# Performance work log

Measured on AMD Instinct MI355X. Metric: run time of the kernel, lower is better.

Reference implementation:

```python
import jax, jax.numpy as jnp
import numpy as np

E2M1_GRID = jnp.array([0.0, 0.5, 1.0, 1.5, 2.0, 3.0, 4.0, 6.0], dtype=jnp.float32)
E2M1_MIDS = (E2M1_GRID[1:] + E2M1_GRID[:-1]) / 2.0
FP4_MAX = 6.0
FP8_E4M3_MAX = 448.0


def nvfp4_quant_dequant(w):
    # Emulates tetrajetv2.quant_fp4_dequant_trans_fused: two-level scaling
    # (fp32 outer scale per 128 inputs, fp8-e4m3 inner scale per 16 inputs),
    # values rounded to the signed E2M1 grid, then dequantized.
    O, I = w.shape
    w16 = w.reshape(O, I // 128, 8, 16)
    amax128 = jnp.max(jnp.abs(w16), axis=(-2, -1))          # [O, I/128]
    outer = amax128 / (FP4_MAX * FP8_E4M3_MAX)
    outer = jnp.where(outer > 0, outer, 1.0)
    amax16 = jnp.max(jnp.abs(w16), axis=-1)                  # [O, I/128, 8]
    inner = amax16 / FP4_MAX / outer[..., None]
    inner = inner.astype(jnp.float8_e4m3fn).astype(jnp.float32)  # fp8 round
    scale = outer[..., None] * inner                          # [O, I/128, 8]
    safe = jnp.where(scale > 0, scale, 1.0)[..., None]
    code = w16 / safe
    a = jnp.abs(code)
    idx = jnp.searchsorted(E2M1_MIDS, a)                      # nearest grid pt
    q = E2M1_GRID[idx] * jnp.sign(code)
    return (q * scale[..., None]).reshape(O, I)


def setup_inputs() -> dict:
    key = jax.random.key(0)
    k0, k1, k2 = jax.random.split(key, 3)
    B, S, H = 2, 2048, 2048
    hidden_states = jax.random.normal(k0, (B, S, H), dtype=jnp.float32)
    # raw weights ~ N(0, 0.023) as in FP4Linear init, then fake-quantized
    w_qkv = jax.random.normal(k1, (3 * H, H), dtype=jnp.float32) * 0.023
    w_o = jax.random.normal(k2, (H, H), dtype=jnp.float32) * 0.023
    w_qkv = nvfp4_quant_dequant(w_qkv)
    w_o = nvfp4_quant_dequant(w_o)
    return {"hidden_states": hidden_states, "w_qkv": w_qkv, "w_o": w_o}


def reference(hidden_states, w_qkv, w_o):
    B, S, H = hidden_states.shape
    num_heads = 16
    head_dim = H // num_heads
    qkv = jnp.einsum('bsh,oh->bso', hidden_states, w_qkv)      # [B,S,3H]
    qkv = qkv.reshape(B, S, 3, num_heads, head_dim)
    qkv = jnp.transpose(qkv, (2, 0, 3, 1, 4))                  # [3,B,nh,S,hd]
    q, k, v = qkv[0], qkv[1], qkv[2]
    scale = 1.0 / jnp.sqrt(jnp.float32(head_dim))
    scores = jnp.einsum('bhqd,bhkd->bhqk', q, k) * scale
    causal = jnp.tril(jnp.ones((S, S), dtype=bool))
    scores = jnp.where(causal, scores, jnp.finfo(scores.dtype).min)
    probs = jax.nn.softmax(scores, axis=-1)
    attn = jnp.einsum('bhqk,bhkd->bhqd', probs, v)             # [B,nh,S,hd]
    attn = jnp.transpose(attn, (0, 2, 1, 3)).reshape(B, S, H)
    return jnp.einsum('bsh,oh->bso', attn, w_o)
```

## Files before the change

kernel.cpp:

```cpp
#include <hip/hip_runtime.h>
#include <hip/hip_bf16.h>
#include <stdint.h>

typedef __bf16 bf16x8 __attribute__((ext_vector_type(8)));
typedef float f32x4 __attribute__((ext_vector_type(4)));

#define AS1 __attribute__((address_space(1)))
#define AS3 __attribute__((address_space(3)))

#define PBAR() do { __builtin_amdgcn_sched_barrier(0); asm volatile("s_barrier" ::: "memory"); __builtin_amdgcn_sched_barrier(0); } while (0)
#define LGK0() do { asm volatile("s_waitcnt lgkmcnt(0)" ::: "memory"); __builtin_amdgcn_sched_barrier(0); } while (0)
#define VMCNT(n) do { asm volatile("s_waitcnt vmcnt(" #n ")" ::: "memory"); __builtin_amdgcn_sched_barrier(0); } while (0)

__device__ __forceinline__ unsigned short f2bf(float x) {
    union { float f; uint32_t u; } v; v.f = x;
    uint32_t r = v.u + 0x7fffu + ((v.u >> 16) & 1u);
    return (unsigned short)(r >> 16);
}

__global__ void k_f2bf(const float* __restrict__ in, unsigned short* __restrict__ out, int n4) {
    int i = blockIdx.x * blockDim.x + threadIdx.x;
    if (i >= n4) return;
    float4 v = reinterpret_cast<const float4*>(in)[i];
    ushort4 o;
    o.x = f2bf(v.x); o.y = f2bf(v.y); o.z = f2bf(v.z); o.w = f2bf(v.w);
    reinterpret_cast<ushort4*>(out)[i] = o;
}

template <typename TOUT>
__global__ __launch_bounds__(512, 2) void k_gemm128x256(
    const unsigned short* __restrict__ A,
    const unsigned short* __restrict__ B,
    TOUT* __restrict__ C, int M, int N, int K, int ngrid)
{
    __shared__ __align__(16) unsigned short Albuf[3][4096];
    __shared__ __align__(16) unsigned short Blbuf[3][8192];
    const int tid = threadIdx.x, lane = tid & 63, wv = tid >> 6;
    const int wr = wv >> 2, wc = wv & 3;
    const int fl = lane & 15, fg = lane >> 4;
    const int cpx = ngrid >> 3;
    const int sw = ((int)blockIdx.x & 7) * cpx + ((int)blockIdx.x >> 3);
    const int bm = sw & 31, bn = sw >> 5;
    const int nK = K >> 5;

    const unsigned short* Ag = A + (size_t)bm * 128 * K;
    const unsigned short* Bg = B + (size_t)bn * 256 * K;

    auto stageA = [&](int buf, int t) {
        const int r = tid >> 2;
        const int cs = (tid & 3) ^ ((r >> 1) & 3);
        const unsigned short* src = Ag + (size_t)r * K + t * 32 + cs * 8;
        __builtin_amdgcn_global_load_lds((const AS1 void*)src,
            (AS3 void*)((char*)&Albuf[buf][0] + wv * 1024), 16, 0, 0);
    };
    auto stageB = [&](int buf, int half, int t) {
        const int r = tid >> 2;
        const int cs = (tid & 3) ^ ((r >> 1) & 3);
        const unsigned short* src = Bg + (size_t)(half * 128 + r) * K + t * 32 + cs * 8;
        __builtin_amdgcn_global_load_lds((const AS1 void*)src,
            (AS3 void*)((char*)&Blbuf[buf][0] + half * 8192 + wv * 1024), 16, 0, 0);
    };
    auto ldfrag = [&](const unsigned short* base, int r) -> bf16x8 {
        return *reinterpret_cast<const bf16x8*>(
            (const char*)base + r * 64 + ((fg ^ ((r >> 1) & 3)) << 4));
    };

    f32x4 acc[4][4];
#pragma unroll
    for (int i = 0; i < 4; ++i)
#pragma unroll
        for (int j = 0; j < 4; ++j) acc[i][j] = (f32x4){0.f, 0.f, 0.f, 0.f};

    stageA(0, 0); stageB(0, 0, 0); stageB(0, 1, 0);
    stageA(1, 1); stageB(1, 0, 1); stageB(1, 1, 1);
    asm volatile("s_waitcnt vmcnt(3)" ::: "memory");
    PBAR();

    int c = 0;
    for (int t = 0; t < nK; ++t) {
        const unsigned short* Ac = Albuf[c];
        const unsigned short* Bc = Blbuf[c];
        bf16x8 af[4], bv[4];
#pragma unroll
        for (int i = 0; i < 4; ++i) af[i] = ldfrag(Ac, wr * 64 + i * 16 + fl);
#pragma unroll
        for (int j = 0; j < 4; ++j) bv[j] = ldfrag(Bc, wc * 64 + j * 16 + fl);
        if (t + 2 < nK) {
            int nb = c + 2; if (nb >= 3) nb -= 3;
            stageA(nb, t + 2); stageB(nb, 0, t + 2); stageB(nb, 1, t + 2);
        }
        PBAR();
        LGK0();
        __builtin_amdgcn_s_setprio(1);
#pragma unroll
        for (int i = 0; i < 4; ++i)
#pragma unroll
            for (int j = 0; j < 4; ++j)
                acc[i][j] = __builtin_amdgcn_mfma_f32_16x16x32_bf16(af[i], bv[j], acc[i][j], 0, 0, 0);
        __builtin_amdgcn_s_setprio(0);
        if (t + 2 < nK)      { asm volatile("s_waitcnt vmcnt(3)" ::: "memory"); }
        else if (t + 1 < nK) { asm volatile("s_waitcnt vmcnt(0)" ::: "memory"); }
        PBAR();
        ++c; if (c == 3) c = 0;
    }

#pragma unroll
    for (int i = 0; i < 4; ++i)
#pragma unroll
        for (int j = 0; j < 4; ++j)
#pragma unroll
            for (int r = 0; r < 4; ++r) {
                int row = bm * 128 + wr * 64 + i * 16 + fg * 4 + r;
                int col = bn * 256 + wc * 64 + j * 16 + fl;
                float v = acc[i][j][r];
                if constexpr (sizeof(TOUT) == 2)
                    ((unsigned short*)C)[(size_t)row * N + col] = f2bf(v);
                else
                    C[(size_t)row * N + col] = v;
            }
}

__global__ void k_transpose_v(const unsigned short* __restrict__ qkv, unsigned short* __restrict__ vT) {
    __shared__ unsigned short t[32][33];
    const int bh = blockIdx.z;
    const int b = bh >> 4, h = bh & 15;
    const int s0 = blockIdx.x * 32, d0 = blockIdx.y * 32;
    const int tx = threadIdx.x, ty = threadIdx.y;
#pragma unroll
    for (int i = 0; i < 4; ++i) {
        int s = s0 + ty + i * 8;
        t[ty + i * 8][tx] = qkv[(size_t)(b * 2048 + s) * 6144 + 4096 + h * 128 + d0 + tx];
    }
    __syncthreads();
#pragma unroll
    for (int i = 0; i < 4; ++i) {
        int d = d0 + ty + i * 8;
        vT[((size_t)bh * 128 + d) * 2048 + s0 + tx] = t[tx][ty + i * 8];
    }
}

__global__ __launch_bounds__(256, 2) void k_attn(
    const unsigned short* __restrict__ qkv, const unsigned short* __restrict__ vT,
    unsigned short* __restrict__ out)
{
    __shared__ unsigned short Klds[2][8192];
    __shared__ unsigned short Vlds[8192];
    __shared__ __align__(16) unsigned short Plds[4][2048];

    const int tid = threadIdx.x, lane = tid & 63, wv = tid >> 6;
    const int fl = lane & 15, fg = lane >> 4;
    const int bh = blockIdx.y;
    const int qb = (bh >= 16) ? blockIdx.x : 15 - blockIdx.x;
    const int b = bh >> 4, h = bh & 15;
    const int q0w = qb * 128 + wv * 32;
    const size_t base = (size_t)b * 2048 * 6144 + (size_t)h * 128;
    const unsigned short* Qbase = qkv + base;
    const unsigned short* Kbase = qkv + base + 2048;
    const unsigned short* Vbase = vT + (size_t)bh * 128 * 2048;
    unsigned short* pw = Plds[wv];

    bf16x8 qf[2][4];
#pragma unroll
    for (int m = 0; m < 2; ++m)
#pragma unroll
        for (int kk = 0; kk < 4; ++kk)
            qf[m][kk] = *reinterpret_cast<const bf16x8*>(
                Qbase + (size_t)(q0w + m * 16 + fl) * 6144 + kk * 32 + fg * 8);
    asm volatile("s_waitcnt vmcnt(0)" ::: "memory");
    __builtin_amdgcn_sched_barrier(0);

    auto stageK = [&](int buf, int kv0) {
#pragma unroll
        for (int rnd = 0; rnd < 4; ++rnd) {
            int ch = rnd * 256 + tid;
            int row = ch >> 4;
            int cbl = ((ch & 15) << 4) ^ ((row & 7) << 4);
            const unsigned short* src = Kbase + (size_t)(kv0 + row) * 6144 + (cbl >> 1);
            __builtin_amdgcn_global_load_lds((const AS1 void*)src,
                (AS3 void*)((char*)&Klds[buf][0] + (rnd * 256 + wv * 64) * 16), 16, 0, 0);
        }
    };
    auto stageV = [&](int kv0) {
#pragma unroll
        for (int rnd = 0; rnd < 4; ++rnd) {
            int ch = rnd * 256 + tid;
            int row = ch >> 3;
            int cbl = ((ch & 7) << 4) ^ ((row & 7) << 4);
            const unsigned short* src = Vbase + (size_t)row * 2048 + kv0 + (cbl >> 1);
            __builtin_amdgcn_global_load_lds((const AS1 void*)src,
                (AS3 void*)((char*)&Vlds[0] + (rnd * 256 + wv * 64) * 16), 16, 0, 0);
        }
    };

    f32x4 acc[2][8];
#pragma unroll
    for (int m = 0; m < 2; ++m)
#pragma unroll
        for (int nb = 0; nb < 8; ++nb) acc[m][nb] = (f32x4){0.f, 0.f, 0.f, 0.f};
    float l_r[2] = {0.f, 0.f};
    const float sc = 0.08838834764831845f;
    const int nIter = 2 * qb + 2;

    stageK(0, 0);

    for (int it = 0; it < nIter; ++it) {
        const int kv0 = it * 64;
        const bool act = (kv0 <= q0w + 31);
        const bool haveK = (it + 1 < nIter);
        stageV(kv0);
        if (haveK) stageK((it + 1) & 1, kv0 + 64);
        __builtin_amdgcn_sched_barrier(0);
        if (haveK) { VMCNT(8); } else { VMCNT(4); }
        PBAR();
        if (act) {
            const bool full = (kv0 + 63 <= q0w);
            const unsigned short* Kb = Klds[it & 1];
            f32x4 s[2][4];
#pragma unroll
            for (int m = 0; m < 2; ++m)
#pragma unroll
                for (int n = 0; n < 4; ++n) s[m][n] = (f32x4){0.f, 0.f, 0.f, 0.f};
            __builtin_amdgcn_s_setprio(1);
#pragma unroll
            for (int kk = 0; kk < 4; ++kk)
#pragma unroll
                for (int n = 0; n < 4; ++n) {
                    const int row = n * 16 + fl;
                    bf16x8 kf = *reinterpret_cast<const bf16x8*>(
                        (const char*)Kb + row * 256 + ((kk * 64 + fg * 16) ^ ((row & 7) << 4)));
                    s[0][n] = __builtin_amdgcn_mfma_f32_16x16x32_bf16(kf, qf[0][kk], s[0][n], 0, 0, 0);
                    s[1][n] = __builtin_amdgcn_mfma_f32_16x16x32_bf16(kf, qf[1][kk], s[1][n], 0, 0, 0);
                }
            __builtin_amdgcn_s_setprio(0);
#pragma unroll
            for (int m = 0; m < 2; ++m) {
                const int qi = q0w + m * 16 + fl;
                const int prow = m * 16 + fl;
                const int rb = prow * 128, swz = (prow & 7) << 4;
#pragma unroll
                for (int n = 0; n < 4; ++n) {
                    const int kbase = kv0 + n * 16 + fg * 4;
                    float v0 = s[m][n][0] * sc, v1 = s[m][n][1] * sc,
                          v2 = s[m][n][2] * sc, v3 = s[m][n][3] * sc;
                    if (!full) {
                        if (kbase     > qi) v0 = -3e38f;
                        if (kbase + 1 > qi) v1 = -3e38f;
                        if (kbase + 2 > qi) v2 = -3e38f;
                        if (kbase + 3 > qi) v3 = -3e38f;
                    }
                    float p0 = __expf(v0 - 10.f), p1 = __expf(v1 - 10.f),
                          p2 = __expf(v2 - 10.f), p3 = __expf(v3 - 10.f);
                    l_r[m] += p0 + p1 + p2 + p3;
                    uint32_t lo = (uint32_t)f2bf(p0) | ((uint32_t)f2bf(p1) << 16);
                    uint32_t hi = (uint32_t)f2bf(p2) | ((uint32_t)f2bf(p3) << 16);
                    const int byte = rb + ((n * 32 + fg * 8) ^ swz);
                    uint2 pk; pk.x = lo; pk.y = hi;
                    *reinterpret_cast<uint2*>((char*)pw + byte) = pk;
                }
            }
            LGK0();
        }
        if (haveK) { VMCNT(4); } else { VMCNT(0); }
        PBAR();
        if (act) {
            bf16x8 pf[2][2];
#pragma unroll
            for (int m = 0; m < 2; ++m)
#pragma unroll
                for (int k2 = 0; k2 < 2; ++k2) {
                    const int row = m * 16 + fl;
                    pf[m][k2] = *reinterpret_cast<const bf16x8*>(
                        (const char*)pw + row * 128 + ((k2 * 64 + fg * 16) ^ ((row & 7) << 4)));
                }
            __builtin_amdgcn_s_setprio(1);
#pragma unroll
            for (int nb = 0; nb < 8; ++nb)
#pragma unroll
                for (int k2 = 0; k2 < 2; ++k2) {
                    const int d = nb * 16 + fl;
                    bf16x8 vf = *reinterpret_cast<const bf16x8*>(
                        (const char*)Vlds + d * 128 + ((k2 * 64 + fg * 16) ^ ((d & 7) << 4)));
                    acc[0][nb] = __builtin_amdgcn_mfma_f32_16x16x32_bf16(pf[0][k2], vf, acc[0][nb], 0, 0, 0);
                    acc[1][nb] = __builtin_amdgcn_mfma_f32_16x16x32_bf16(pf[1][k2], vf, acc[1][nb], 0, 0, 0);
                }
            __builtin_amdgcn_s_setprio(0);
        }
        PBAR();
    }

#pragma unroll
    for (int m = 0; m < 2; ++m) {
        float l = l_r[m];
        l += __shfl_xor(l, 16);
        l += __shfl_xor(l, 32);
        float inv[4];
#pragma unroll
        for (int r = 0; r < 4; ++r) inv[r] = 1.0f / __shfl(l, fg * 4 + r);
#pragma unroll
        for (int nb = 0; nb < 8; ++nb)
#pragma unroll
            for (int r = 0; r < 4; ++r) {
                int row = q0w + m * 16 + fg * 4 + r;
                int col = h * 128 + nb * 16 + fl;
                out[(size_t)(b * 2048 + row) * 2048 + col] = f2bf(acc[m][nb][r] * inv[r]);
            }
    }
}

extern "C" void kernel_launch(void* const* d_in, const int* in_sizes, int n_in,
                              void* d_out, int out_size, void* d_ws, size_t ws_size,
                              hipStream_t stream) {
    const float* hs   = (const float*)d_in[0];
    const float* wqkv = (const float*)d_in[1];
    const float* wo   = (const float*)d_in[2];
    float* out = (float*)d_out;

    char* p = (char*)d_ws;
    unsigned short* Xb    = (unsigned short*)p; p += (size_t)4096 * 2048 * 2;
    unsigned short* Wqkvb = (unsigned short*)p; p += (size_t)6144 * 2048 * 2;
    unsigned short* Wob   = (unsigned short*)p; p += (size_t)2048 * 2048 * 2;
    unsigned short* QKV   = (unsigned short*)p; p += (size_t)4096 * 6144 * 2;
    unsigned short* VT    = (unsigned short*)p; p += (size_t)32 * 128 * 2048 * 2;
    unsigned short* ATTN  = (unsigned short*)p; p += (size_t)4096 * 2048 * 2;

    k_f2bf<<<8192, 256, 0, stream>>>(hs, Xb, 2097152);
    k_f2bf<<<12288, 256, 0, stream>>>(wqkv, Wqkvb, 3145728);
    k_f2bf<<<4096, 256, 0, stream>>>(wo, Wob, 1048576);
    k_gemm128x256<unsigned short><<<768, 512, 0, stream>>>(Xb, Wqkvb, QKV, 4096, 6144, 2048, 768);
    k_transpose_v<<<dim3(64, 4, 32), dim3(32, 8), 0, stream>>>(QKV, VT);
    k_attn<<<dim3(16, 32), 256, 0, stream>>>(QKV, VT, ATTN);
    k_gemm128x256<float><<<256, 512, 0, stream>>>(ATTN, Wob, out, 4096, 2048, 2048, 256);
}
```

Measured before the change: 263.0 us.

## Fuse bf16 conversions, shrink GEMM tiles to 128x128, use exp2 in softmax

Merges the three fp32-to-bf16 conversion launches into one kernel, cutting launch overhead. Both GEMMs move from 128x256 tiles with 512 threads to 128x128 tiles with 256 threads and three blocks per CU. This doubles the grid, which should give better CU occupancy and tail balance, but it lowers operand reuse per tile. The attention softmax folds log2(e) into the scale and calls the hardware exp2 directly.

New measurement: 264.9 us. Within noise of the previous version (+0.7%).

```diff
diff --git a/kernel.cpp b/kernel.cpp
--- a/kernel.cpp
+++ b/kernel.cpp
@@ -18,47 +18,58 @@
     return (unsigned short)(r >> 16);
 }
 
-__global__ void k_f2bf(const float* __restrict__ in, unsigned short* __restrict__ out, int n4) {
+__global__ void k_f2bf3(const float* __restrict__ a, unsigned short* __restrict__ oa, int na4,
+                        const float* __restrict__ b, unsigned short* __restrict__ ob, int nb4,
+                        const float* __restrict__ c, unsigned short* __restrict__ oc, int nc4) {
     int i = blockIdx.x * blockDim.x + threadIdx.x;
-    if (i >= n4) return;
-    float4 v = reinterpret_cast<const float4*>(in)[i];
+    const float* src; unsigned short* dst; int j;
+    if (i < na4)            { src = a; dst = oa; j = i; }
+    else if (i < na4 + nb4) { src = b; dst = ob; j = i - na4; }
+    else if (i < na4 + nb4 + nc4) { src = c; dst = oc; j = i - na4 - nb4; }
+    else return;
+    float4 v = reinterpret_cast<const float4*>(src)[j];
     ushort4 o;
     o.x = f2bf(v.x); o.y = f2bf(v.y); o.z = f2bf(v.z); o.w = f2bf(v.w);
-    reinterpret_cast<ushort4*>(out)[i] = o;
+    reinterpret_cast<ushort4*>(dst)[j] = o;
 }
 
 template <typename TOUT>
-__global__ __launch_bounds__(512, 2) void k_gemm128x256(
+__global__ __launch_bounds__(256, 3) void k_gemm128x128(
     const unsigned short* __restrict__ A,
     const unsigned short* __restrict__ B,
     TOUT* __restrict__ C, int M, int N, int K, int ngrid)
 {
-    __shared__ __align__(16) unsigned short Albuf[3][4096];
-    __shared__ __align__(16) unsigned short Blbuf[3][8192];
+    __shared__ __align__(16) unsigned short Al[3][4096];
+    __shared__ __align__(16) unsigned short Bl[3][4096];
     const int tid = threadIdx.x, lane = tid & 63, wv = tid >> 6;
-    const int wr = wv >> 2, wc = wv & 3;
+    const int wr = wv >> 1, wc = wv & 1;
     const int fl = lane & 15, fg = lane >> 4;
+    const int nbm = M >> 7;
     const int cpx = ngrid >> 3;
     const int sw = ((int)blockIdx.x & 7) * cpx + ((int)blockIdx.x >> 3);
-    const int bm = sw & 31, bn = sw >> 5;
+    const int bm = sw % nbm, bn = sw / nbm;
     const int nK = K >> 5;
 
     const unsigned short* Ag = A + (size_t)bm * 128 * K;
-    const unsigned short* Bg = B + (size_t)bn * 256 * K;
-
-    auto stageA = [&](int buf, int t) {
-        const int r = tid >> 2;
-        const int cs = (tid & 3) ^ ((r >> 1) & 3);
-        const unsigned short* src = Ag + (size_t)r * K + t * 32 + cs * 8;
-        __builtin_amdgcn_global_load_lds((const AS1 void*)src,
-            (AS3 void*)((char*)&Albuf[buf][0] + wv * 1024), 16, 0, 0);
-    };
-    auto stageB = [&](int buf, int half, int t) {
-        const int r = tid >> 2;
-        const int cs = (tid & 3) ^ ((r >> 1) & 3);
-        const unsigned short* src = Bg + (size_t)(half * 128 + r) * K + t * 32 + cs * 8;
-        __builtin_amdgcn_global_load_lds((const AS1 void*)src,
-            (AS3 void*)((char*)&Blbuf[buf][0] + half * 8192 + wv * 1024), 16, 0, 0);
+    const unsigned short* Bg = B + (size_t)bn * 128 * K;
+
+    auto stage = [&](int buf, int t) {
+#pragma unroll
+        for (int u = 0; u < 2; ++u) {
+            int ch = u * 256 + tid;
+            int r = ch >> 2, cs = (ch & 3) ^ ((r >> 1) & 3);
+            __builtin_amdgcn_global_load_lds(
+                (const AS1 void*)(Ag + (size_t)r * K + t * 32 + cs * 8),
+                (AS3 void*)((char*)&Al[buf][0] + (u * 256 + wv * 64) * 16), 16, 0, 0);
+        }
+#pragma unroll
+        for (int u = 0; u < 2; ++u) {
+            int ch = u * 256 + tid;
+            int r = ch >> 2, cs = (ch & 3) ^ ((r >> 1) & 3);
+            __builtin_amdgcn_global_load_lds(
+                (const AS1 void*)(Bg + (size_t)r * K + t * 32 + cs * 8),
+                (AS3 void*)((char*)&Bl[buf][0] + (u * 256 + wv * 64) * 16), 16, 0, 0);
+        }
     };
     auto ldfrag = [&](const unsigned short* base, int r) -> bf16x8 {
         return *reinterpret_cast<const bf16x8*>(
@@ -71,15 +82,15 @@
 #pragma unroll
         for (int j = 0; j < 4; ++j) acc[i][j] = (f32x4){0.f, 0.f, 0.f, 0.f};
 
-    stageA(0, 0); stageB(0, 0, 0); stageB(0, 1, 0);
-    stageA(1, 1); stageB(1, 0, 1); stageB(1, 1, 1);
-    asm volatile("s_waitcnt vmcnt(3)" ::: "memory");
+    stage(0, 0);
+    stage(1, 1);
+    asm volatile("s_waitcnt vmcnt(4)" ::: "memory");
     PBAR();
 
     int c = 0;
     for (int t = 0; t < nK; ++t) {
-        const unsigned short* Ac = Albuf[c];
-        const unsigned short* Bc = Blbuf[c];
+        const unsigned short* Ac = Al[c];
+        const unsigned short* Bc = Bl[c];
         bf16x8 af[4], bv[4];
 #pragma unroll
         for (int i = 0; i < 4; ++i) af[i] = ldfrag(Ac, wr * 64 + i * 16 + fl);
@@ -87,7 +98,7 @@
         for (int j = 0; j < 4; ++j) bv[j] = ldfrag(Bc, wc * 64 + j * 16 + fl);
         if (t + 2 < nK) {
             int nb = c + 2; if (nb >= 3) nb -= 3;
-            stageA(nb, t + 2); stageB(nb, 0, t + 2); stageB(nb, 1, t + 2);
+            stage(nb, t + 2);
         }
         PBAR();
         LGK0();
@@ -98,7 +109,7 @@
             for (int j = 0; j < 4; ++j)
                 acc[i][j] = __builtin_amdgcn_mfma_f32_16x16x32_bf16(af[i], bv[j], acc[i][j], 0, 0, 0);
         __builtin_amdgcn_s_setprio(0);
-        if (t + 2 < nK)      { asm volatile("s_waitcnt vmcnt(3)" ::: "memory"); }
+        if (t + 2 < nK)      { asm volatile("s_waitcnt vmcnt(4)" ::: "memory"); }
         else if (t + 1 < nK) { asm volatile("s_waitcnt vmcnt(0)" ::: "memory"); }
         PBAR();
         ++c; if (c == 3) c = 0;
@@ -111,7 +122,7 @@
 #pragma unroll
             for (int r = 0; r < 4; ++r) {
                 int row = bm * 128 + wr * 64 + i * 16 + fg * 4 + r;
-                int col = bn * 256 + wc * 64 + j * 16 + fl;
+                int col = bn * 128 + wc * 64 + j * 16 + fl;
                 float v = acc[i][j][r];
                 if constexpr (sizeof(TOUT) == 2)
                     ((unsigned short*)C)[(size_t)row * N + col] = f2bf(v);
@@ -198,7 +209,8 @@
 #pragma unroll
         for (int nb = 0; nb < 8; ++nb) acc[m][nb] = (f32x4){0.f, 0.f, 0.f, 0.f};
     float l_r[2] = {0.f, 0.f};
-    const float sc = 0.08838834764831845f;
+    const float sc2 = 0.12751879523473098f;
+    const float c2  = 14.426950408889634f;
     const int nIter = 2 * qb + 2;
 
     stageK(0, 0);
@@ -240,16 +252,16 @@
 #pragma unroll
                 for (int n = 0; n < 4; ++n) {
                     const int kbase = kv0 + n * 16 + fg * 4;
-                    float v0 = s[m][n][0] * sc, v1 = s[m][n][1] * sc,
-                          v2 = s[m][n][2] * sc, v3 = s[m][n][3] * sc;
+                    float v0 = s[m][n][0] * sc2, v1 = s[m][n][1] * sc2,
+                          v2 = s[m][n][2] * sc2, v3 = s[m][n][3] * sc2;
                     if (!full) {
                         if (kbase     > qi) v0 = -3e38f;
                         if (kbase + 1 > qi) v1 = -3e38f;
                         if (kbase + 2 > qi) v2 = -3e38f;
                         if (kbase + 3 > qi) v3 = -3e38f;
                     }
-                    float p0 = __expf(v0 - 10.f), p1 = __expf(v1 - 10.f),
-                          p2 = __expf(v2 - 10.f), p3 = __expf(v3 - 10.f);
+                    float p0 = __builtin_amdgcn_exp2f(v0 - c2), p1 = __builtin_amdgcn_exp2f(v1 - c2),
+                          p2 = __builtin_amdgcn_exp2f(v2 - c2), p3 = __builtin_amdgcn_exp2f(v3 - c2);
                     l_r[m] += p0 + p1 + p2 + p3;
                     uint32_t lo = (uint32_t)f2bf(p0) | ((uint32_t)f2bf(p1) << 16);
                     uint32_t hi = (uint32_t)f2bf(p2) | ((uint32_t)f2bf(p3) << 16);
@@ -323,11 +335,9 @@
     unsigned short* VT    = (unsigned short*)p; p += (size_t)32 * 128 * 2048 * 2;
     unsigned short* ATTN  = (unsigned short*)p; p += (size_t)4096 * 2048 * 2;
 
-    k_f2bf<<<8192, 256, 0, stream>>>(hs, Xb, 2097152);
-    k_f2bf<<<12288, 256, 0, stream>>>(wqkv, Wqkvb, 3145728);
-    k_f2bf<<<4096, 256, 0, stream>>>(wo, Wob, 1048576);
-    k_gemm128x256<unsigned short><<<768, 512, 0, stream>>>(Xb, Wqkvb, QKV, 4096, 6144, 2048, 768);
+    k_f2bf3<<<24576, 256, 0, stream>>>(hs, Xb, 2097152, wqkv, Wqkvb, 3145728, wo, Wob, 1048576);
+    k_gemm128x128<unsigned short><<<1536, 256, 0, stream>>>(Xb, Wqkvb, QKV, 4096, 6144, 2048, 1536);
     k_transpose_v<<<dim3(64, 4, 32), dim3(32, 8), 0, stream>>>(QKV, VT);
     k_attn<<<dim3(16, 32), 256, 0, stream>>>(QKV, VT, ATTN);
-    k_gemm128x256<float><<<256, 512, 0, stream>>>(ATTN, Wob, out, 4096, 2048, 2048, 256);
-}
+    k_gemm128x128<float><<<512, 256, 0, stream>>>(ATTN, Wob, out, 4096, 2048, 2048, 512);
+}
```
